# Optimization experiments

Measured on AMD Instinct MI355X. Metric: run time of the kernel, lower is better.

The kernel has to match this reference:

```python
import jax, jax.numpy as jnp
import numpy as np

P = 32; H = 4; D_MODEL = 512; N_LAYER = 4; D_STATE = 16; D_CONV = 4; EXPAND = 2
D_INNER = EXPAND * D_MODEL        # 1024
DT_RANK = D_MODEL // 16           # 32 (ceil(512/16))
B_SZ, L_SEQ = 8, 2048


def _ln(x, w, b):
    mu = jnp.mean(x, axis=-1, keepdims=True)
    var = jnp.mean(jnp.square(x - mu), axis=-1, keepdims=True)
    return (x - mu) * jax.lax.rsqrt(var + 1e-5) * w + b


def _selective_scan(xc, dt, A, Bm, Cm, Dskip):
    # xc, dt: (B,L,D); Bm, Cm: (B,L,N); A: (D,N); Dskip: (D,)
    def step(h, inp):
        dt_t, b_t, c_t, x_t = inp                      # (B,D),(B,N),(B,N),(B,D)
        dA = jnp.exp(dt_t[:, :, None] * A)             # (B,D,N)
        h = dA * h + (dt_t * x_t)[:, :, None] * b_t[:, None, :]
        y = jnp.einsum('bdn,bn->bd', h, c_t)
        return h, y
    h0 = jnp.zeros((xc.shape[0], xc.shape[2], A.shape[1]), xc.dtype)
    xs = (jnp.swapaxes(dt, 0, 1), jnp.swapaxes(Bm, 0, 1),
          jnp.swapaxes(Cm, 0, 1), jnp.swapaxes(xc, 0, 1))
    _, ys = jax.lax.scan(step, h0, xs)
    return jnp.swapaxes(ys, 0, 1) + xc * Dskip


def _mamba_block(h, ln_w, ln_b, mix_w, conv_w, conv_b, xproj_w,
                 dtproj_w, dtproj_b, A_log, Dskip, out_w):
    L = h.shape[1]
    xin = _ln(h, ln_w, ln_b)
    xz = xin @ mix_w.T                                  # (B,L,2*D_INNER)
    x, z = jnp.split(xz, 2, axis=-1)
    # causal depthwise conv1d (kernel D_CONV)
    xpad = jnp.pad(x, ((0, 0), (D_CONV - 1, 0), (0, 0)))
    xc = conv_b + sum(conv_w[:, k] * xpad[:, k:k + L] for k in range(D_CONV))
    xc = jax.nn.silu(xc)
    dbl = xc @ xproj_w.T                                # (B,L,DT_RANK+2*N)
    dt_r, Bm, Cm = jnp.split(dbl, [DT_RANK, DT_RANK + D_STATE], axis=-1)
    dt = jax.nn.softplus(dt_r @ dtproj_w.T + dtproj_b)  # (B,L,D_INNER)
    A = -jnp.exp(A_log)                                 # (D_INNER, N)
    y = _selective_scan(xc, dt, A, Bm, Cm, Dskip)
    y = y * jax.nn.silu(z)
    return h + y @ out_w.T


def setup_inputs() -> dict:
    key = jax.random.key(0)
    ks = jax.random.split(key, 12)
    def rn(k, shape, scale=0.02):
        return jax.random.normal(k, shape, jnp.float32) * scale
    A_init = jnp.log(jnp.arange(1, D_STATE + 1, dtype=jnp.float32))
    return {
        'y': jax.random.normal(ks[0], (B_SZ, L_SEQ, P), jnp.float32),
        'emb_w': rn(ks[1], (D_MODEL, P)), 'emb_b': jnp.zeros((D_MODEL,), jnp.float32),
        'ln_w': jnp.ones((N_LAYER, D_MODEL), jnp.float32),
        'ln_b': jnp.zeros((N_LAYER, D_MODEL), jnp.float32),
        'mix_w': rn(ks[2], (N_LAYER, 2 * D_INNER, D_MODEL)),
        'conv_w': rn(ks[3], (N_LAYER, D_INNER, D_CONV), 0.2),
        'conv_b': jnp.zeros((N_LAYER, D_INNER), jnp.float32),
        'xproj_w': rn(ks[4], (N_LAYER, DT_RANK + 2 * D_STATE, D_INNER)),
        'dtproj_w': rn(ks[5], (N_LAYER, D_INNER, DT_RANK), 0.1),
        'dtproj_b': jnp.full((N_LAYER, D_INNER), -4.6, jnp.float32),
        'A_log': jnp.tile(A_init[None, None, :], (N_LAYER, D_INNER, 1)),
        'Dskip': jnp.ones((N_LAYER, D_INNER), jnp.float32),
        'out_w': rn(ks[6], (N_LAYER, D_MODEL, D_INNER)),
        'normf_w': jnp.ones((D_MODEL,), jnp.float32),
        'normf_b': jnp.zeros((D_MODEL,), jnp.float32),
        'ro1_w': rn(ks[7], (D_MODEL, D_MODEL)), 'ro1_b': jnp.zeros((D_MODEL,), jnp.float32),
        'ro2_w': rn(ks[8], (H * P, D_MODEL)), 'ro2_b': jnp.zeros((H * P,), jnp.float32),
    }


def reference(y, emb_w, emb_b, ln_w, ln_b, mix_w, conv_w, conv_b, xproj_w,
              dtproj_w, dtproj_b, A_log, Dskip, out_w, normf_w, normf_b,
              ro1_w, ro1_b, ro2_w, ro2_b):
    B, L, _ = y.shape
    h = y @ emb_w.T + emb_b                             # (B,L,D_MODEL)
    for i in range(N_LAYER):
        h = _mamba_block(h, ln_w[i], ln_b[i], mix_w[i], conv_w[i], conv_b[i],
                         xproj_w[i], dtproj_w[i], dtproj_b[i], A_log[i],
                         Dskip[i], out_w[i])
    h = _ln(h, normf_w, normf_b)
    h = jax.nn.gelu(h @ ro1_w.T + ro1_b)
    out = h @ ro2_w.T + ro2_b                           # (B,L,H*P)
    return out.reshape(B, L, H, P)
```

## Files before the change

kernel.cpp:

```cpp
#include <hip/hip_runtime.h>
#include <hip/hip_bf16.h>
#include <math.h>

#define B_SZ 8
#define L_SEQ 2048
#define TOK (B_SZ * L_SEQ)
#define D_MODEL 512
#define D_INNER 1024
#define N_LAYER 4
#define D_STATE 16
#define D_CONV 4
#define DT_RANK 32

#define LC 64
#define NCH (L_SEQ / LC)

typedef __attribute__((ext_vector_type(8))) short short8;
typedef __attribute__((ext_vector_type(4))) float floatx4;

__device__ __forceinline__ unsigned short f2bs(float x) {
    unsigned int u = __float_as_uint(x);
    unsigned int r = (u + 0x7FFFu + ((u >> 16) & 1u)) >> 16;
    return (unsigned short)r;
}
__device__ __forceinline__ float bs2f(unsigned short s) {
    return __uint_as_float(((unsigned int)s) << 16);
}

__device__ __forceinline__ float softplus_f(float x) {
    float u = __expf(-fabsf(x));
    return fmaxf(x, 0.0f) + __logf(1.0f + u);
}
__device__ __forceinline__ float gelu_f(float x) {
    float u2 = 1.5957691216057308f * (x + 0.044715f * x * x * x);
    return x / (1.0f + __expf(-u2));
}

#define POW16(av, p)                                                   \
    av[0] = (p);                                                       \
    av[1] = av[0] * av[0];                                             \
    av[3] = av[1] * av[1];                                             \
    av[7] = av[3] * av[3];                                             \
    av[15] = av[7] * av[7];                                            \
    av[2] = av[1] * av[0];                                             \
    av[4] = av[3] * av[0];                                             \
    av[5] = av[3] * av[1];                                             \
    av[6] = av[3] * av[2];                                             \
    av[8]  = av[7] * av[0];                                            \
    av[9]  = av[7] * av[1];                                            \
    av[10] = av[7] * av[2];                                            \
    av[11] = av[7] * av[3];                                            \
    av[12] = av[7] * av[4];                                            \
    av[13] = av[7] * av[5];                                            \
    av[14] = av[7] * av[6];

__global__ __launch_bounds__(256) void cvt_bf16(
    const float* __restrict__ in, unsigned short* __restrict__ out, int n4)
{
    int i = blockIdx.x * 256 + threadIdx.x;
    if (i < n4) {
        float4 v = ((const float4*)in)[i];
        ushort4 u;
        u.x = f2bs(v.x); u.y = f2bs(v.y); u.z = f2bs(v.z); u.w = f2bs(v.w);
        ((ushort4*)out)[i] = u;
    }
}

__device__ __forceinline__ void gload_lds16(const void* g, void* l) {
    __builtin_amdgcn_global_load_lds(
        (const __attribute__((address_space(1))) unsigned int*)g,
        (__attribute__((address_space(3))) unsigned int*)l, 16, 0, 0);
}

#define VMW(n)  asm volatile("s_waitcnt vmcnt(" #n ")" ::: "memory")
#define LGKM0() asm volatile("s_waitcnt lgkmcnt(0)" ::: "memory")
#define SBAR()  asm volatile("s_barrier" ::: "memory")


__device__ __forceinline__ void stage_slot8p(
    const unsigned short* __restrict__ A,
    const unsigned short* __restrict__ W,
    unsigned short* __restrict__ sm,
    int slot, int row0, int col0, int k0, int w, int lane)
{
    unsigned short* sp = sm + slot * 16384;
#pragma unroll
    for (int r = 0; r < 2; ++r) {
        const int c   = r * 512 + w * 64 + lane;
        const int row = c >> 2;
        const int kc  = (c & 3) ^ ((row >> 1) & 3);
        gload_lds16(A + (size_t)(row0 + row) * 512 + (k0 + kc * 8),
                    sp + (size_t)(r * 512 + w * 64) * 8);
        gload_lds16(W + (size_t)(col0 + row) * 512 + (k0 + kc * 8),
                    sp + 8192 + (size_t)(r * 512 + w * 64) * 8);
    }
}

__global__ __launch_bounds__(512, 2) void gemm_mix_8p(
    const unsigned short* __restrict__ A,
    const unsigned short* __restrict__ W,
    unsigned short* __restrict__ X,
    unsigned short* __restrict__ Z)
{
    __shared__ __align__(16) unsigned short sm[4 * 16384];

    const int tid  = threadIdx.x;
    const int lane = tid & 63;
    const int w    = tid >> 6;
    const int wm   = w >> 2;
    const int wn   = w & 3;
    const int m    = lane & 15;
    const int quad = (lane >> 4) & 3;
    const int kx   = (quad ^ ((m >> 1) & 3)) * 8;

    const int bid  = blockIdx.x;
    const int swz  = (bid & 7) * 64 + (bid >> 3);
    const int row0 = (swz >> 3) * 256;
    const int col0 = (swz & 7) * 256;

    floatx4 acc[8][4];
#pragma unroll
    for (int i = 0; i < 8; ++i)
#pragma unroll
        for (int j = 0; j < 4; ++j) { floatx4 zz = {0.f,0.f,0.f,0.f}; acc[i][j] = zz; }

    stage_slot8p(A, W, sm, 0, row0, col0, 0,  w, lane);
    stage_slot8p(A, W, sm, 1, row0, col0, 32, w, lane);
    stage_slot8p(A, W, sm, 2, row0, col0, 64, w, lane);

#pragma unroll
    for (int t = 0; t < 16; ++t) {
        if (t + 3 < 16)
            stage_slot8p(A, W, sm, (t + 3) & 3, row0, col0, (t + 3) * 32, w, lane);
        if (t < 13)       VMW(12);
        else if (t == 13) VMW(8);
        else if (t == 14) VMW(4);
        else              VMW(0);
        SBAR();

        const unsigned short* as = sm + (t & 3) * 16384
                                   + (size_t)(wm * 128 + m) * 32 + kx;
        const unsigned short* bs = sm + (t & 3) * 16384 + 8192
                                   + (size_t)(wn * 64 + m) * 32 + kx;

        short8 af[4], bf[4];
#pragma unroll
        for (int i = 0; i < 4; ++i) af[i] = *(const short8*)(as + i * 512);
#pragma unroll
        for (int j = 0; j < 4; ++j) bf[j] = *(const short8*)(bs + j * 512);
        SBAR();
        LGKM0();
        __builtin_amdgcn_sched_barrier(0);
        __builtin_amdgcn_s_setprio(1);
#pragma unroll
        for (int i = 0; i < 4; ++i)
#pragma unroll
            for (int j = 0; j < 4; ++j)
                acc[i][j] = __builtin_amdgcn_mfma_f32_16x16x32_bf16(
                    af[i], bf[j], acc[i][j], 0, 0, 0);
        __builtin_amdgcn_s_setprio(0);

        short8 ag[4];
#pragma unroll
        for (int i = 0; i < 4; ++i) ag[i] = *(const short8*)(as + 2048 + i * 512);
        SBAR();
        LGKM0();
        __builtin_amdgcn_sched_barrier(0);
        __builtin_amdgcn_s_setprio(1);
#pragma unroll
        for (int i = 0; i < 4; ++i)
#pragma unroll
            for (int j = 0; j < 4; ++j)
                acc[4 + i][j] = __builtin_amdgcn_mfma_f32_16x16x32_bf16(
                    ag[i], bf[j], acc[4 + i][j], 0, 0, 0);
        __builtin_amdgcn_s_setprio(0);
        SBAR();
    }

    unsigned short* dst; int dcol0;
    if (col0 >= 1024) { dst = Z; dcol0 = col0 - 1024; }
    else              { dst = X; dcol0 = col0; }
#pragma unroll
    for (int h = 0; h < 2; ++h) {
        __syncthreads();
        if (wm == h) {
#pragma unroll
            for (int i = 0; i < 8; ++i)
#pragma unroll
                for (int j = 0; j < 4; ++j) {
                    const int lc = wn * 64 + j * 16 + m;
#pragma unroll
                    for (int r = 0; r < 4; ++r)
                        sm[(i * 16 + quad * 4 + r) * 264 + lc] =
                            f2bs(acc[i][j][r]);
                }
        }
        __syncthreads();
#pragma unroll
        for (int p = 0; p < 8; ++p) {
            const int idx = p * 512 + tid;
            const int row = idx >> 5, ch = (idx & 31) * 8;
            short8 v = *(const short8*)&sm[row * 264 + ch];
            *(short8*)(dst + (size_t)(row0 + h * 128 + row) * 1024 + dcol0 + ch) = v;
        }
    }
}

#define EPAD 168

__device__ __forceinline__ void stage_slot128(
    const unsigned short* __restrict__ A,
    const unsigned short* __restrict__ W,
    unsigned short* __restrict__ sm,
    int slot, int row0, int col0, int k0, int K, int w, int lane)
{
    unsigned short* sp = sm + slot * 8192;
#pragma unroll
    for (int r = 0; r < 2; ++r) {
        const int c   = r * 256 + w * 64 + lane;
        const int row = c >> 2;
        const int kc  = (c & 3) ^ ((row >> 1) & 3);
        gload_lds16(A + (size_t)(row0 + row) * K + (k0 + kc * 8),
                    sp + (size_t)(r * 256 + w * 64) * 8);
        gload_lds16(W + (size_t)(col0 + row) * K + (k0 + kc * 8),
                    sp + 4096 + (size_t)(r * 256 + w * 64) * 8);
    }
}

__device__ __forceinline__ void gemm128_core(
    const unsigned short* __restrict__ A,
    const unsigned short* __restrict__ W,
    unsigned short* __restrict__ sm,
    floatx4 (&acc)[4][4],
    int row0, int col0, int K, int w, int lane)
{
    const int wm = w & 1, wn = w >> 1;
    const int m = lane & 15, quad = (lane >> 4) & 3;
    const int kx = (quad ^ ((m >> 1) & 3)) * 8;

    const int NT = K >> 5;
    stage_slot128(A, W, sm, 0, row0, col0, 0,  K, w, lane);
    stage_slot128(A, W, sm, 1, row0, col0, 32, K, w, lane);
    stage_slot128(A, W, sm, 2, row0, col0, 64, K, w, lane);

    for (int t = 0; t < NT; ++t) {
        if (t + 3 < NT)
            stage_slot128(A, W, sm, (t + 3) & 3, row0, col0, (t + 3) * 32, K, w, lane);
        if (t < NT - 3)       VMW(12);
        else if (t == NT - 3) VMW(8);
        else if (t == NT - 2) VMW(4);
        else                  VMW(0);
        SBAR();

        const unsigned short* as = sm + (t & 3) * 8192
                                   + (size_t)(wm * 64 + m) * 32 + kx;
        const unsigned short* bs = sm + (t & 3) * 8192 + 4096
                                   + (size_t)(wn * 64 + m) * 32 + kx;

        short8 af[4], bf[4];
#pragma unroll
        for (int i = 0; i < 4; ++i) af[i] = *(const short8*)(as + i * 512);
#pragma unroll
        for (int j = 0; j < 4; ++j) bf[j] = *(const short8*)(bs + j * 512);
        SBAR();
        LGKM0();
        __builtin_amdgcn_sched_barrier(0);
        __builtin_amdgcn_s_setprio(1);
#pragma unroll
        for (int i = 0; i < 4; ++i)
#pragma unroll
            for (int j = 0; j < 4; ++j)
                acc[i][j] = __builtin_amdgcn_mfma_f32_16x16x32_bf16(
                    af[i], bf[j], acc[i][j], 0, 0, 0);
        __builtin_amdgcn_s_setprio(0);
        SBAR();
    }
}

__global__ __launch_bounds__(256, 2) void gemm_res128_8p(
    const unsigned short* __restrict__ A,
    const unsigned short* __restrict__ W,
    unsigned short* __restrict__ HR,
    int K)
{
    __shared__ __align__(16) unsigned short sm[4 * 8192];

    const int tid  = threadIdx.x;
    const int lane = tid & 63;
    const int w    = tid >> 6;
    const int wm   = w & 1, wn = w >> 1;
    const int m    = lane & 15, quad = (lane >> 4) & 3;

    const int bid  = blockIdx.x;
    const int swz  = (bid & 7) * 64 + (bid >> 3);
    const int row0 = (swz >> 2) * 128;
    const int col0 = (swz & 3) * 128;

    floatx4 acc[4][4];
#pragma unroll
    for (int i = 0; i < 4; ++i)
#pragma unroll
        for (int j = 0; j < 4; ++j) { floatx4 zz = {0.f,0.f,0.f,0.f}; acc[i][j] = zz; }

    gemm128_core(A, W, sm, acc, row0, col0, K, w, lane);

    unsigned short* Es = sm;
#pragma unroll
    for (int h = 0; h < 2; ++h) {
        __syncthreads();
        if (wm == h) {
#pragma unroll
            for (int i = 0; i < 4; ++i)
#pragma unroll
                for (int j = 0; j < 4; ++j) {
                    const int lcol = wn * 64 + j * 16 + m;
#pragma unroll
                    for (int r = 0; r < 4; ++r)
                        Es[(i * 16 + quad * 4 + r) * EPAD + lcol] =
                            f2bs(acc[i][j][r]);
                }
        }
        __syncthreads();
#pragma unroll
        for (int p = 0; p < 4; ++p) {
            const int idx = p * 256 + tid;
            const int row = idx >> 4, colc = (idx & 15) * 8;
            short8 vv = *(const short8*)&Es[row * EPAD + colc];
            size_t goff = (size_t)(row0 + h * 64 + row) * 512 + col0 + colc;
            short8 rv = *(const short8*)(HR + goff);
#pragma unroll
            for (int e = 0; e < 8; ++e)
                vv[e] = (short)f2bs(bs2f((unsigned short)vv[e]) +
                                    bs2f((unsigned short)rv[e]));
            *(short8*)(HR + goff) = vv;
        }
    }
}

__global__ __launch_bounds__(256, 2) void gemm_head_8p(
    const unsigned short* __restrict__ A,
    const unsigned short* __restrict__ W,
    const float* __restrict__ bias,
    float* __restrict__ G)
{
    __shared__ __align__(16) unsigned short sm[4 * 8192];

    const int tid  = threadIdx.x;
    const int lane = tid & 63;
    const int w    = tid >> 6;
    const int wm   = w & 1, wn = w >> 1;
    const int m    = lane & 15, quad = (lane >> 4) & 3;

    const int bid  = blockIdx.x;
    const int swz  = (bid & 7) * 64 + (bid >> 3);
    const int row0 = (swz >> 2) * 128;
    const int col0 = (swz & 3) * 128;

    floatx4 acc[4][4];
#pragma unroll
    for (int i = 0; i < 4; ++i)
#pragma unroll
        for (int j = 0; j < 4; ++j) { floatx4 zz = {0.f,0.f,0.f,0.f}; acc[i][j] = zz; }

    gemm128_core(A, W, sm, acc, row0, col0, 512, w, lane);

    float* Ef = (float*)sm;
#pragma unroll
    for (int h = 0; h < 2; ++h) {
        __syncthreads();
        if (wm == h) {
#pragma unroll
            for (int i = 0; i < 4; ++i)
#pragma unroll
                for (int j = 0; j < 4; ++j) {
                    const int lcol = wn * 64 + j * 16 + m;
                    const float bv = bias[col0 + lcol];
#pragma unroll
                    for (int r = 0; r < 4; ++r)
                        Ef[(i * 16 + quad * 4 + r) * 132 + lcol] =
                            gelu_f(acc[i][j][r] + bv);
                }
        }
        __syncthreads();
#pragma unroll
        for (int p = 0; p < 8; ++p) {
            const int idx = p * 256 + tid;
            const int row = idx >> 5, c4 = (idx & 31) * 4;
            float4 v = *(const float4*)&Ef[row * 132 + c4];
            *(float4*)(G + (size_t)(row0 + h * 64 + row) * 512 + col0 + c4) = v;
        }
    }
}

#define BM 64
#define BN 64
#define BK 16

__global__ __launch_bounds__(256) void gemm_f32(
    const float* __restrict__ A, int lda,
    const float* __restrict__ W,
    const float* __restrict__ bias,
    const float* res,
    void* Cv, int M, int N, int K, int act, int bf16out)
{
    __shared__ float As[BK][BM + 4];
    __shared__ float Ws[BK][BN + 4];

    const int tid = threadIdx.x;
    const int tx = tid & 15;
    const int ty = tid >> 4;
    const int row0 = blockIdx.y * BM;
    const int col0 = blockIdx.x * BN;

    const int lr = tid >> 2;
    const int lk = (tid & 3) * 4;

    float acc[4][4];
#pragma unroll
    for (int i = 0; i < 4; ++i)
#pragma unroll
        for (int j = 0; j < 4; ++j) acc[i][j] = 0.0f;

    const float* Aptr = A + (size_t)(row0 + lr) * lda + lk;
    const float* Wptr = W + (size_t)(col0 + lr) * K + lk;

    for (int k0 = 0; k0 < K; k0 += BK) {
        float4 av = *(const float4*)(Aptr + k0);
        float4 wv = *(const float4*)(Wptr + k0);
        __syncthreads();
        As[lk + 0][lr] = av.x; As[lk + 1][lr] = av.y;
        As[lk + 2][lr] = av.z; As[lk + 3][lr] = av.w;
        Ws[lk + 0][lr] = wv.x; Ws[lk + 1][lr] = wv.y;
        Ws[lk + 2][lr] = wv.z; Ws[lk + 3][lr] = wv.w;
        __syncthreads();
#pragma unroll
        for (int k = 0; k < BK; ++k) {
            float4 a4 = *(const float4*)&As[k][ty * 4];
            float4 w4 = *(const float4*)&Ws[k][tx * 4];
            float a[4] = {a4.x, a4.y, a4.z, a4.w};
            float wv2[4] = {w4.x, w4.y, w4.z, w4.w};
#pragma unroll
            for (int i = 0; i < 4; ++i)
#pragma unroll
                for (int j = 0; j < 4; ++j)
                    acc[i][j] = fmaf(a[i], wv2[j], acc[i][j]);
        }
    }

    float4 bv = make_float4(0.f, 0.f, 0.f, 0.f);
    if (bias) bv = *(const float4*)(bias + col0 + tx * 4);
#pragma unroll
    for (int i = 0; i < 4; ++i) {
        int r = row0 + ty * 4 + i;
        size_t off = (size_t)r * N + col0 + tx * 4;
        float4 v = make_float4(acc[i][0] + bv.x, acc[i][1] + bv.y,
                               acc[i][2] + bv.z, acc[i][3] + bv.w);
        if (res) {
            float4 rv = *(const float4*)(res + off);
            v.x += rv.x; v.y += rv.y; v.z += rv.z; v.w += rv.w;
        }
        if (act == 1) {
            v.x = softplus_f(v.x); v.y = softplus_f(v.y);
            v.z = softplus_f(v.z); v.w = softplus_f(v.w);
        }
        if (bf16out) {
            ushort4 u;
            u.x = f2bs(v.x); u.y = f2bs(v.y); u.z = f2bs(v.z); u.w = f2bs(v.w);
            *(ushort4*)((unsigned short*)Cv + off) = u;
        } else {
            *(float4*)((float*)Cv + off) = v;
        }
    }
}

__global__ __launch_bounds__(256) void gemm_f32_sk64(
    const unsigned short* __restrict__ A16, const float* __restrict__ W,
    float* __restrict__ Cp)
{
    __shared__ float As[BK][BM + 4];
    __shared__ float Ws[BK][BN + 4];

    const int s    = blockIdx.x;
    const int row0 = blockIdx.y * BM;
    const int tid = threadIdx.x;
    const int tx = tid & 15;
    const int ty = tid >> 4;
    const int lr = tid >> 2;
    const int lk = (tid & 3) * 4;

    float acc[4][4];
#pragma unroll
    for (int i = 0; i < 4; ++i)
#pragma unroll
        for (int j = 0; j < 4; ++j) acc[i][j] = 0.0f;

    const unsigned short* Aptr = A16 + (size_t)(row0 + lr) * D_INNER + s * 256 + lk;
    const float* Wptr = W + (size_t)lr * D_INNER + s * 256 + lk;

    for (int k0 = 0; k0 < 256; k0 += BK) {
        ushort4 av = *(const ushort4*)(Aptr + k0);
        float4 wv = *(const float4*)(Wptr + k0);
        __syncthreads();
        As[lk + 0][lr] = bs2f(av.x); As[lk + 1][lr] = bs2f(av.y);
        As[lk + 2][lr] = bs2f(av.z); As[lk + 3][lr] = bs2f(av.w);
        Ws[lk + 0][lr] = wv.x; Ws[lk + 1][lr] = wv.y;
        Ws[lk + 2][lr] = wv.z; Ws[lk + 3][lr] = wv.w;
        __syncthreads();
#pragma unroll
        for (int k = 0; k < BK; ++k) {
            float4 a4 = *(const float4*)&As[k][ty * 4];
            float4 w4 = *(const float4*)&Ws[k][tx * 4];
            float a[4] = {a4.x, a4.y, a4.z, a4.w};
            float wv2[4] = {w4.x, w4.y, w4.z, w4.w};
#pragma unroll
            for (int i = 0; i < 4; ++i)
#pragma unroll
                for (int j = 0; j < 4; ++j)
                    acc[i][j] = fmaf(a[i], wv2[j], acc[i][j]);
        }
    }

#pragma unroll
    for (int i = 0; i < 4; ++i) {
        size_t off = ((size_t)s * TOK + row0 + ty * 4 + i) * 64 + tx * 4;
        *(float4*)(Cp + off) = make_float4(acc[i][0], acc[i][1],
                                           acc[i][2], acc[i][3]);
    }
}

__global__ __launch_bounds__(256) void reduce4_64(
    const float* __restrict__ Cp, float* __restrict__ dbl)
{
    int i = blockIdx.x * 256 + threadIdx.x;
    const float4* p = (const float4*)Cp;
    float4 a = p[i];
    float4 b = p[i + (TOK * 64) / 4];
    float4 c = p[i + 2 * (TOK * 64) / 4];
    float4 d = p[i + 3 * (TOK * 64) / 4];
    float4 o;
    o.x = (a.x + b.x) + (c.x + d.x);
    o.y = (a.y + b.y) + (c.y + d.y);
    o.z = (a.z + b.z) + (c.z + d.z);
    o.w = (a.w + b.w) + (c.w + d.w);
    ((float4*)dbl)[i] = o;
}

__global__ __launch_bounds__(256) void ln_kernel(
    const unsigned short* __restrict__ x, const float* __restrict__ w,
    const float* __restrict__ b, unsigned short* __restrict__ o)
{
    const int tok = blockIdx.x;
    const int tid = threadIdx.x;
    const unsigned short* xp = x + (size_t)tok * D_MODEL;

    ushort2 u = *(const ushort2*)(xp + tid * 2);
    float vx = bs2f(u.x), vy = bs2f(u.y);
    float s = vx + vy;
    float ss = vx * vx + vy * vy;
#pragma unroll
    for (int off = 32; off > 0; off >>= 1) {
        s  += __shfl_down(s, off);
        ss += __shfl_down(ss, off);
    }
    __shared__ float sh[10];
    int wid = tid >> 6;
    if ((tid & 63) == 0) { sh[wid] = s; sh[4 + wid] = ss; }
    __syncthreads();
    if (tid == 0) {
        float S = sh[0] + sh[1] + sh[2] + sh[3];
        float SS = sh[4] + sh[5] + sh[6] + sh[7];
        float mu = S * (1.0f / D_MODEL);
        float var = SS * (1.0f / D_MODEL) - mu * mu;
        sh[8] = mu;
        sh[9] = rsqrtf(var + 1e-5f);
    }
    __syncthreads();
    float mu = sh[8], rs = sh[9];
    float2 wv = *(const float2*)(w + tid * 2);
    float2 bv = *(const float2*)(b + tid * 2);
    ushort2 ov;
    ov.x = f2bs((vx - mu) * rs * wv.x + bv.x);
    ov.y = f2bs((vy - mu) * rs * wv.y + bv.y);
    *(ushort2*)(o + (size_t)tok * D_MODEL + tid * 2) = ov;
}

#define CT 8
__global__ __launch_bounds__(256) void conv_silu(
    const unsigned short* __restrict__ x16, const float* __restrict__ cw,
    const float* __restrict__ cb, unsigned short* __restrict__ xc16)
{
    const int tid = threadIdx.x;
    const int d8 = (tid & 127) * 8;
    const size_t tok0 = (size_t)blockIdx.x * (2 * CT) + (size_t)(tid >> 7) * CT;
    const int l0 = (int)(tok0 & (L_SEQ - 1));

    float4 taps[8];
#pragma unroll
    for (int j = 0; j < 8; ++j) taps[j] = ((const float4*)cw)[d8 + j];
    float bias[8];
    {
        float4 b0 = ((const float4*)cb)[d8 >> 2];
        float4 b1 = ((const float4*)cb)[(d8 >> 2) + 1];
        bias[0] = b0.x; bias[1] = b0.y; bias[2] = b0.z; bias[3] = b0.w;
        bias[4] = b1.x; bias[5] = b1.y; bias[6] = b1.z; bias[7] = b1.w;
    }

    const short8* xp = (const short8*)(x16 + tok0 * D_INNER + d8);
    short8*       op = (short8*)(xc16 + tok0 * D_INNER + d8);

    float wm3[8], wm2[8], wm1[8];
    if (l0 > 0) {
        short8 a3 = xp[-3 * 128], a2 = xp[-2 * 128], a1 = xp[-1 * 128];
#pragma unroll
        for (int j = 0; j < 8; ++j) {
            wm3[j] = bs2f((unsigned short)a3[j]);
            wm2[j] = bs2f((unsigned short)a2[j]);
            wm1[j] = bs2f((unsigned short)a1[j]);
        }
    } else {
#pragma unroll
        for (int j = 0; j < 8; ++j) { wm3[j] = 0.f; wm2[j] = 0.f; wm1[j] = 0.f; }
    }

#pragma unroll
    for (int t = 0; t < CT; ++t) {
        short8 cv = xp[t * 128];
        float cur[8];
#pragma unroll
        for (int j = 0; j < 8; ++j) cur[j] = bs2f((unsigned short)cv[j]);
        short8 out;
#pragma unroll
        for (int j = 0; j < 8; ++j) {
            float a = bias[j];
            a = fmaf(taps[j].x, wm3[j], a);
            a = fmaf(taps[j].y, wm2[j], a);
            a = fmaf(taps[j].z, wm1[j], a);
            a = fmaf(taps[j].w, cur[j], a);
            float s = a / (1.0f + __expf(-a));
            out[j] = (short)f2bs(s);
        }
        op[t * 128] = out;
#pragma unroll
        for (int j = 0; j < 8; ++j) { wm3[j] = wm2[j]; wm2[j] = wm1[j]; wm1[j] = cur[j]; }
    }
}

__global__ __launch_bounds__(256) void scan_phase1(
    const unsigned short* __restrict__ dt16,
    const unsigned short* __restrict__ xc16,
    const float* __restrict__ dbl,
    float* __restrict__ sdtbuf, float* __restrict__ Sbuf)
{
    __shared__ __align__(16) float sB[LC][16];

    const int bid = blockIdx.x;
    const int tid = threadIdx.x;
    const int d = ((bid & 3) << 8) + tid;
    const int bc = bid >> 2;
    const size_t tok0 = (size_t)bc * LC;

    {
        int t = tid >> 2, j = tid & 3;
        ((float4*)&sB[t][0])[j] =
            ((const float4*)dbl)[(tok0 + t) * 16 + 8 + j];
    }
    __syncthreads();

    float hs[16];
#pragma unroll
    for (int n = 0; n < 16; ++n) hs[n] = 0.0f;
    float sdt = 0.0f;

    const unsigned short* dp = dt16 + tok0 * D_INNER + d;
    const unsigned short* xp = xc16 + tok0 * D_INNER + d;

#pragma unroll 2
    for (int l = 0; l < LC; ++l) {
        float dtv = bs2f(dp[(size_t)l * D_INNER]);
        float xv  = bs2f(xp[(size_t)l * D_INNER]);
        float dtx = dtv * xv;
        sdt += dtv;
        float av[16];
        float p = __expf(-dtv);
        POW16(av, p);
        const float4* Bp = (const float4*)&sB[l][0];
#pragma unroll
        for (int q = 0; q < 4; ++q) {
            float4 bv = Bp[q];
            hs[q*4+0] = fmaf(av[q*4+0], hs[q*4+0], dtx * bv.x);
            hs[q*4+1] = fmaf(av[q*4+1], hs[q*4+1], dtx * bv.y);
            hs[q*4+2] = fmaf(av[q*4+2], hs[q*4+2], dtx * bv.z);
            hs[q*4+3] = fmaf(av[q*4+3], hs[q*4+3], dtx * bv.w);
        }
    }
    const int gcd = (bc << 10) + d;
    float4* Sp = (float4*)(Sbuf + (size_t)gcd * D_STATE);
#pragma unroll
    for (int q = 0; q < 4; ++q) Sp[q] = ((float4*)hs)[q];
    sdtbuf[gcd] = sdt;
}

__global__ __launch_bounds__(256) void scan_phase2(
    const float* __restrict__ sdtbuf, const float* __restrict__ A_log,
    float* __restrict__ Sbuf)
{
    const int g = blockIdx.x * 256 + threadIdx.x;
    const int n = g & (D_STATE - 1);
    const int d = (g >> 4) & (D_INNER - 1);
    const int b = g >> 14;

    const float An = -__expf(A_log[d * D_STATE + n]);
    float E = 0.0f;
#pragma unroll 4
    for (int c = 0; c < NCH; ++c) {
        const int gcd = ((b * NCH + c) << 10) + d;
        float P = __expf(An * sdtbuf[gcd]);
        size_t idx = ((size_t)gcd * D_STATE) + n;
        float S = Sbuf[idx];
        Sbuf[idx] = E;
        E = fmaf(P, E, S);
    }
}

__global__ __launch_bounds__(256) void scan_phase3(
    const unsigned short* __restrict__ dt16,
    const unsigned short* __restrict__ xc16,
    const float* __restrict__ dbl,
    const float* __restrict__ Dsk,
    unsigned short* __restrict__ yz16,
    const float* __restrict__ Sbuf)
{
    __shared__ __align__(16) float sBC[LC][32];

    const int bid = blockIdx.x;
    const int tid = threadIdx.x;
    const int d = ((bid & 3) << 8) + tid;
    const int bc = bid >> 2;
    const size_t tok0 = (size_t)bc * LC;

#pragma unroll
    for (int q = 0; q < 2; ++q) {
        int idx = tid + q * 256;
        int t = idx >> 3, j = idx & 7;
        ((float4*)&sBC[t][0])[j] =
            ((const float4*)dbl)[(tok0 + t) * 16 + 8 + j];
    }
    __syncthreads();

    float hs[16];
    const int gcd = (bc << 10) + d;
    const float4* Sp = (const float4*)(Sbuf + (size_t)gcd * D_STATE);
#pragma unroll
    for (int q = 0; q < 4; ++q) ((float4*)hs)[q] = Sp[q];
    const float Dv = Dsk[d];

    const unsigned short* dp = dt16 + tok0 * D_INNER + d;
    const unsigned short* xp = xc16 + tok0 * D_INNER + d;
    unsigned short*       yp = yz16 + tok0 * D_INNER + d;

#pragma unroll 2
    for (int l = 0; l < LC; ++l) {
        float dtv = bs2f(dp[(size_t)l * D_INNER]);
        float xv  = bs2f(xp[(size_t)l * D_INNER]);
        float zv  = bs2f(yp[(size_t)l * D_INNER]);
        float dtx = dtv * xv;
        float av[16];
        float p = __expf(-dtv);
        POW16(av, p);
        const float4* Bp = (const float4*)&sBC[l][0];
        float y = 0.0f;
#pragma unroll
        for (int q = 0; q < 4; ++q) {
            float4 bv = Bp[q];
            float4 cv = Bp[4 + q];
            hs[q*4+0] = fmaf(av[q*4+0], hs[q*4+0], dtx * bv.x);
            y = fmaf(hs[q*4+0], cv.x, y);
            hs[q*4+1] = fmaf(av[q*4+1], hs[q*4+1], dtx * bv.y);
            y = fmaf(hs[q*4+1], cv.y, y);
            hs[q*4+2] = fmaf(av[q*4+2], hs[q*4+2], dtx * bv.z);
            y = fmaf(hs[q*4+2], cv.z, y);
            hs[q*4+3] = fmaf(av[q*4+3], hs[q*4+3], dtx * bv.w);
            y = fmaf(hs[q*4+3], cv.w, y);
        }
        y = fmaf(xv, Dv, y);
        float sig = 1.0f / (1.0f + __expf(-zv));
        y *= zv * sig;
        yp[(size_t)l * D_INNER] = f2bs(y);
    }
}

extern "C" void kernel_launch(void* const* d_in, const int* in_sizes, int n_in,
                              void* d_out, int out_size, void* d_ws, size_t ws_size,
                              hipStream_t stream)
{
    const float* y_in     = (const float*)d_in[0];
    const float* emb_w    = (const float*)d_in[1];
    const float* emb_b    = (const float*)d_in[2];
    const float* ln_w     = (const float*)d_in[3];
    const float* ln_b     = (const float*)d_in[4];
    const float* mix_w    = (const float*)d_in[5];
    const float* conv_w   = (const float*)d_in[6];
    const float* conv_b   = (const float*)d_in[7];
    const float* xproj_w  = (const float*)d_in[8];
    const float* dtproj_w = (const float*)d_in[9];
    const float* dtproj_b = (const float*)d_in[10];
    const float* A_log    = (const float*)d_in[11];
    const float* Dskip    = (const float*)d_in[12];
    const float* out_w    = (const float*)d_in[13];
    const float* normf_w  = (const float*)d_in[14];
    const float* normf_b  = (const float*)d_in[15];
    const float* ro1_w    = (const float*)d_in[16];
    const float* ro1_b    = (const float*)d_in[17];
    const float* ro2_w    = (const float*)d_in[18];
    const float* ro2_b    = (const float*)d_in[19];

    char* base = (char*)d_ws;
    unsigned short* h16   = (unsigned short*)(base);
    unsigned short* xin16 = (unsigned short*)(base + 33554432);
    unsigned short* x16   = (unsigned short*)(base + 67108864);
    unsigned short* xc16  = (unsigned short*)(base + 100663296);
    unsigned short* dt16  = (unsigned short*)(base + 134217728);
    unsigned short* z16   = (unsigned short*)(base + 167772160);
    float*          dbl   = (float*)(base + 201326592);
    float*          sdtb  = (float*)(base + 205520896);
    float*          Sbuf  = (float*)(base + 206569472);
    float*          dbl4  = (float*)(base + 206569472);
    unsigned short* mw16  = (unsigned short*)(base + 223346688);
    unsigned short* ow16  = (unsigned short*)(base + 231735296);
    unsigned short* r1w16 = (unsigned short*)(base + 235929600);
    float*          g1    = (float*)(base + 100663296);

    const int M = TOK;
    const int scan_blocks = (B_SZ * NCH * D_INNER) / 256;

    {
        int n4 = (N_LAYER * 2 * D_INNER * D_MODEL) / 4;
        cvt_bf16<<<(n4 + 255) / 256, 256, 0, stream>>>(mix_w, mw16, n4);
        n4 = (N_LAYER * D_MODEL * D_INNER) / 4;
        cvt_bf16<<<(n4 + 255) / 256, 256, 0, stream>>>(out_w, ow16, n4);
        n4 = (D_MODEL * D_MODEL) / 4;
        cvt_bf16<<<(n4 + 255) / 256, 256, 0, stream>>>(ro1_w, r1w16, n4);
    }

    gemm_f32<<<dim3(D_MODEL / BN, M / BM), 256, 0, stream>>>(
        y_in, 32, emb_w, emb_b, nullptr, h16, M, D_MODEL, 32, 0, 1);

    for (int i = 0; i < N_LAYER; ++i) {
        const unsigned short* mwl = mw16 + (size_t)i * 2 * D_INNER * D_MODEL;

        ln_kernel<<<M, 256, 0, stream>>>(h16, ln_w + i * D_MODEL, ln_b + i * D_MODEL, xin16);

        gemm_mix_8p<<<512, 512, 0, stream>>>(xin16, mwl, x16, z16);

        conv_silu<<<TOK / (2 * CT), 256, 0, stream>>>(
            x16, conv_w + i * D_INNER * D_CONV, conv_b + i * D_INNER, xc16);

        gemm_f32_sk64<<<dim3(4, M / BM), 256, 0, stream>>>(
            xc16, xproj_w + (size_t)i * 64 * D_INNER, dbl4);
        reduce4_64<<<(TOK * 64 / 4) / 256, 256, 0, stream>>>(dbl4, dbl);

        gemm_f32<<<dim3(D_INNER / BN, M / BM), 256, 0, stream>>>(
            dbl, 64, dtproj_w + (size_t)i * D_INNER * DT_RANK,
            dtproj_b + i * D_INNER, nullptr, dt16, M, D_INNER, DT_RANK, 1, 1);

        const float* Al = A_log + (size_t)i * D_INNER * D_STATE;
        scan_phase1<<<scan_blocks, 256, 0, stream>>>(dt16, xc16, dbl, sdtb, Sbuf);
        scan_phase2<<<(B_SZ * D_INNER * D_STATE) / 256, 256, 0, stream>>>(sdtb, Al, Sbuf);
        scan_phase3<<<scan_blocks, 256, 0, stream>>>(
            dt16, xc16, dbl, Dskip + i * D_INNER, z16, Sbuf);

        gemm_res128_8p<<<512, 256, 0, stream>>>(
            z16, ow16 + (size_t)i * D_MODEL * D_INNER, h16, D_INNER);
    }

    ln_kernel<<<M, 256, 0, stream>>>(h16, normf_w, normf_b, xin16);
    gemm_head_8p<<<512, 256, 0, stream>>>(xin16, r1w16, ro1_b, g1);
    gemm_f32<<<dim3(128 / BN, M / BM), 256, 0, stream>>>(
        g1, D_MODEL, ro2_w, ro2_b, nullptr, d_out, M, 128, D_MODEL, 0, 0);

    (void)in_sizes; (void)n_in; (void)out_size; (void)ws_size;
}
```

Baseline: 1.219 ms.

## Run x_proj GEMM on bf16 MFMA with pipelined LDS staging

Replaces the FP32 FMA split-K x_proj GEMM with a bf16 MFMA kernel that uses a 4-slot async global-to-LDS pipeline and swizzled shared-memory layout. The x_proj weights are converted to bf16 once up front into a new workspace region. The aim is to cut the CUDA-core FMA cost of this per-layer projection, at the price of bf16 rounding of the weights and possible overlap risk with the chosen workspace offset.

Measured after the change: 1.085 ms. 1.12x faster.

```diff
diff --git a/kernel.cpp b/kernel.cpp
--- a/kernel.cpp
+++ b/kernel.cpp
@@ -392,6 +392,103 @@
     }
 }
 
+__device__ __forceinline__ void stage_xp(
+    const unsigned short* __restrict__ A,
+    const unsigned short* __restrict__ W,
+    unsigned short* __restrict__ sm,
+    int slot, int row0, int k0, int w, int lane)
+{
+    unsigned short* sp = sm + slot * 6144;
+#pragma unroll
+    for (int r = 0; r < 2; ++r) {
+        const int c   = r * 256 + w * 64 + lane;
+        const int row = c >> 2;
+        const int kc  = (c & 3) ^ ((row >> 1) & 3);
+        gload_lds16(A + (size_t)(row0 + row) * D_INNER + (k0 + kc * 8),
+                    sp + (size_t)(r * 256 + w * 64) * 8);
+    }
+    {
+        const int c   = w * 64 + lane;
+        const int row = c >> 2;
+        const int kc  = (c & 3) ^ ((row >> 1) & 3);
+        gload_lds16(W + (size_t)row * D_INNER + (k0 + kc * 8),
+                    sp + 4096 + (size_t)(w * 64) * 8);
+    }
+}
+
+__global__ __launch_bounds__(256, 2) void gemm_xproj_8p(
+    const unsigned short* __restrict__ A,
+    const unsigned short* __restrict__ W,
+    float* __restrict__ Cp)
+{
+    __shared__ __align__(16) unsigned short sm[4 * 6144];
+
+    const int tid  = threadIdx.x;
+    const int lane = tid & 63;
+    const int w    = tid >> 6;
+    const int m    = lane & 15, quad = (lane >> 4) & 3;
+    const int kx   = (quad ^ ((m >> 1) & 3)) * 8;
+
+    const int bid  = blockIdx.x;
+    const int s    = bid & 3;
+    const int row0 = (bid >> 2) * 128;
+    const int k0s  = s * 256;
+
+    floatx4 acc[2][4];
+#pragma unroll
+    for (int i = 0; i < 2; ++i)
+#pragma unroll
+        for (int j = 0; j < 4; ++j) { floatx4 zz = {0.f,0.f,0.f,0.f}; acc[i][j] = zz; }
+
+    stage_xp(A, W, sm, 0, row0, k0s + 0,  w, lane);
+    stage_xp(A, W, sm, 1, row0, k0s + 32, w, lane);
+    stage_xp(A, W, sm, 2, row0, k0s + 64, w, lane);
+
+#pragma unroll
+    for (int t = 0; t < 8; ++t) {
+        if (t + 3 < 8)
+            stage_xp(A, W, sm, (t + 3) & 3, row0, k0s + (t + 3) * 32, w, lane);
+        if (t < 5)       VMW(9);
+        else if (t == 5) VMW(6);
+        else if (t == 6) VMW(3);
+        else             VMW(0);
+        SBAR();
+
+        const unsigned short* as = sm + (t & 3) * 6144
+                                   + (size_t)(w * 32 + m) * 32 + kx;
+        const unsigned short* bs = sm + (t & 3) * 6144 + 4096
+                                   + (size_t)m * 32 + kx;
+
+        short8 af[2], bf[4];
+#pragma unroll
+        for (int i = 0; i < 2; ++i) af[i] = *(const short8*)(as + i * 512);
+#pragma unroll
+        for (int j = 0; j < 4; ++j) bf[j] = *(const short8*)(bs + j * 512);
+        SBAR();
+        LGKM0();
+        __builtin_amdgcn_sched_barrier(0);
+        __builtin_amdgcn_s_setprio(1);
+#pragma unroll
+        for (int i = 0; i < 2; ++i)
+#pragma unroll
+            for (int j = 0; j < 4; ++j)
+                acc[i][j] = __builtin_amdgcn_mfma_f32_16x16x32_bf16(
+                    af[i], bf[j], acc[i][j], 0, 0, 0);
+        __builtin_amdgcn_s_setprio(0);
+        SBAR();
+    }
+
+    float* cp = Cp + ((size_t)s * TOK + row0) * 64;
+#pragma unroll
+    for (int i = 0; i < 2; ++i)
+#pragma unroll
+        for (int j = 0; j < 4; ++j)
+#pragma unroll
+            for (int r = 0; r < 4; ++r)
+                cp[(size_t)(w * 32 + i * 16 + quad * 4 + r) * 64 + j * 16 + m] =
+                    acc[i][j][r];
+}
+
 #define BM 64
 #define BN 64
 #define BK 16
@@ -470,61 +567,6 @@
         } else {
             *(float4*)((float*)Cv + off) = v;
         }
-    }
-}
-
-__global__ __launch_bounds__(256) void gemm_f32_sk64(
-    const unsigned short* __restrict__ A16, const float* __restrict__ W,
-    float* __restrict__ Cp)
-{
-    __shared__ float As[BK][BM + 4];
-    __shared__ float Ws[BK][BN + 4];
-
-    const int s    = blockIdx.x;
-    const int row0 = blockIdx.y * BM;
-    const int tid = threadIdx.x;
-    const int tx = tid & 15;
-    const int ty = tid >> 4;
-    const int lr = tid >> 2;
-    const int lk = (tid & 3) * 4;
-
-    float acc[4][4];
-#pragma unroll
-    for (int i = 0; i < 4; ++i)
-#pragma unroll
-        for (int j = 0; j < 4; ++j) acc[i][j] = 0.0f;
-
-    const unsigned short* Aptr = A16 + (size_t)(row0 + lr) * D_INNER + s * 256 + lk;
-    const float* Wptr = W + (size_t)lr * D_INNER + s * 256 + lk;
-
-    for (int k0 = 0; k0 < 256; k0 += BK) {
-        ushort4 av = *(const ushort4*)(Aptr + k0);
-        float4 wv = *(const float4*)(Wptr + k0);
-        __syncthreads();
-        As[lk + 0][lr] = bs2f(av.x); As[lk + 1][lr] = bs2f(av.y);
-        As[lk + 2][lr] = bs2f(av.z); As[lk + 3][lr] = bs2f(av.w);
-        Ws[lk + 0][lr] = wv.x; Ws[lk + 1][lr] = wv.y;
-        Ws[lk + 2][lr] = wv.z; Ws[lk + 3][lr] = wv.w;
-        __syncthreads();
-#pragma unroll
-        for (int k = 0; k < BK; ++k) {
-            float4 a4 = *(const float4*)&As[k][ty * 4];
-            float4 w4 = *(const float4*)&Ws[k][tx * 4];
-            float a[4] = {a4.x, a4.y, a4.z, a4.w};
-            float wv2[4] = {w4.x, w4.y, w4.z, w4.w};
-#pragma unroll
-            for (int i = 0; i < 4; ++i)
-#pragma unroll
-                for (int j = 0; j < 4; ++j)
-                    acc[i][j] = fmaf(a[i], wv2[j], acc[i][j]);
-        }
-    }
-
-#pragma unroll
-    for (int i = 0; i < 4; ++i) {
-        size_t off = ((size_t)s * TOK + row0 + ty * 4 + i) * 64 + tx * 4;
-        *(float4*)(Cp + off) = make_float4(acc[i][0], acc[i][1],
-                                           acc[i][2], acc[i][3]);
     }
 }
 
@@ -816,6 +858,7 @@
 
     char* base = (char*)d_ws;
     unsigned short* h16   = (unsigned short*)(base);
+    unsigned short* xw16  = (unsigned short*)(base + 16777216);
     unsigned short* xin16 = (unsigned short*)(base + 33554432);
     unsigned short* x16   = (unsigned short*)(base + 67108864);
     unsigned short* xc16  = (unsigned short*)(base + 100663296);
@@ -840,6 +883,8 @@
         cvt_bf16<<<(n4 + 255) / 256, 256, 0, stream>>>(out_w, ow16, n4);
         n4 = (D_MODEL * D_MODEL) / 4;
         cvt_bf16<<<(n4 + 255) / 256, 256, 0, stream>>>(ro1_w, r1w16, n4);
+        n4 = (N_LAYER * 64 * D_INNER) / 4;
+        cvt_bf16<<<(n4 + 255) / 256, 256, 0, stream>>>(xproj_w, xw16, n4);
     }
 
     gemm_f32<<<dim3(D_MODEL / BN, M / BM), 256, 0, stream>>>(
@@ -855,8 +900,8 @@
         conv_silu<<<TOK / (2 * CT), 256, 0, stream>>>(
             x16, conv_w + i * D_INNER * D_CONV, conv_b + i * D_INNER, xc16);
 
-        gemm_f32_sk64<<<dim3(4, M / BM), 256, 0, stream>>>(
-            xc16, xproj_w + (size_t)i * 64 * D_INNER, dbl4);
+        gemm_xproj_8p<<<512, 256, 0, stream>>>(
+            xc16, xw16 + (size_t)i * 64 * D_INNER, dbl4);
         reduce4_64<<<(TOK * 64 / 4) / 256, 256, 0, stream>>>(dbl4, dbl);
 
         gemm_f32<<<dim3(D_INNER / BN, M / BM), 256, 0, stream>>>(
```
